# Kernel tuning notes

Hardware: AMD Instinct MI355X
Metric: run time of the kernel (lower is better)

## Reference

```python
import jax, jax.numpy as jnp
import numpy as np

B, S, T, E, H, F = 2, 2048, 2048, 1024, 16, 4096
HD = E // H
EPS = 1e-5


def setup_inputs() -> dict:
    key = jax.random.key(0)
    ks = jax.random.split(key, 16)
    def w(k, shape):
        return (jax.random.normal(k, shape, jnp.float32) * 0.02)
    d = {
        "x": jax.random.normal(ks[0], (B, S, E), jnp.float32),
        "enc": jax.random.normal(ks[1], (B, T, E), jnp.float32),
    }
    for i, n in enumerate(["sa_q", "sa_k", "sa_v", "sa_o", "ca_q", "ca_k", "ca_v", "ca_o"]):
        d[n + "w"] = w(ks[2 + i], (E, E))  # torch Linear: [out, in]
        d[n + "b"] = jnp.zeros((E,), jnp.float32)
    d["w1"] = w(ks[10], (F, E)); d["b1"] = jnp.zeros((F,), jnp.float32)
    d["w2"] = w(ks[11], (E, F)); d["b2"] = jnp.zeros((E,), jnp.float32)
    for n in ["ln1", "ln2", "ln3"]:
        d[n + "_g"] = jnp.ones((E,), jnp.float32)
        d[n + "_b"] = jnp.zeros((E,), jnp.float32)
    return d


def _layernorm(x, g, b):
    m = jnp.mean(x, axis=-1, keepdims=True)
    v = jnp.mean((x - m) ** 2, axis=-1, keepdims=True)
    return (x - m) / jnp.sqrt(v + EPS) * g + b


def _heads(x, w, b):
    bsz, sl, _ = x.shape
    y = x @ w.T + b
    return y.reshape(bsz, sl, H, HD).transpose(0, 2, 1, 3)  # [B,H,S,hd]


def _mha(xq, xkv, qw, qb, kw, kb, vw, vb, ow, ob, causal):
    q = _heads(xq, qw, qb)
    k = _heads(xkv, kw, kb)
    v = _heads(xkv, vw, vb)
    scores = jnp.einsum('bhsd,bhtd->bhst', q, k) / np.sqrt(HD).astype(np.float32)
    if causal:
        sl, tl = scores.shape[-2], scores.shape[-1]
        mask = jnp.tril(jnp.ones((sl, tl), bool))
        scores = jnp.where(mask, scores, -jnp.inf)
    a = jax.nn.softmax(scores, axis=-1)
    o = jnp.einsum('bhst,bhtd->bhsd', a, v)
    o = o.transpose(0, 2, 1, 3).reshape(xq.shape[0], xq.shape[1], E)
    return o @ ow.T + ob


def reference(x, enc,
              sa_qw, sa_qb, sa_kw, sa_kb, sa_vw, sa_vb, sa_ow, sa_ob,
              ca_qw, ca_qb, ca_kw, ca_kb, ca_vw, ca_vb, ca_ow, ca_ob,
              w1, b1, w2, b2,
              ln1_g, ln1_b, ln2_g, ln2_b, ln3_g, ln3_b):
    sa = _mha(x, x, sa_qw, sa_qb, sa_kw, sa_kb, sa_vw, sa_vb, sa_ow, sa_ob, True)
    x = _layernorm(x + sa, ln1_g, ln1_b)
    ca = _mha(x, enc, ca_qw, ca_qb, ca_kw, ca_kb, ca_vw, ca_vb, ca_ow, ca_ob, False)
    x = _layernorm(x + ca, ln2_g, ln2_b)
    ffn = jax.nn.relu(x @ w1.T + b1) @ w2.T + b2
    return _layernorm(x + ffn, ln3_g, ln3_b)
```

## Files before the change

### kernel.cpp

```cpp
#include <hip/hip_runtime.h>
#include <hip/hip_bf16.h>
#include <stdint.h>

typedef __attribute__((ext_vector_type(8))) short s16x8;
typedef __attribute__((ext_vector_type(4))) short s16x4;
typedef __attribute__((ext_vector_type(4))) float f32x4;

#define DEV static __device__ __forceinline__

DEV ushort f2bu(float f){
  unsigned u = __builtin_bit_cast(unsigned, f);
  return (ushort)((u + 0x7fffu + ((u >> 16) & 1u)) >> 16);
}
DEV ushort f2bn(float f){
  return __builtin_bit_cast(ushort, __float2bfloat16(f));
}

DEV void gload16(const void* g, void* l){
  __builtin_amdgcn_global_load_lds((const __attribute__((address_space(1))) void*)g,
                                   (__attribute__((address_space(3))) void*)l, 16, 0, 0);
}

struct ConvArgs {
  const float* src[17];
  void*        dst[17];
  int blk_end[17];
  int nel[17];
  unsigned f32mask;
};

__global__ void __launch_bounds__(256) k_conv(ConvArgs a){
  int bi = blockIdx.x, seg = 0;
  while (bi >= a.blk_end[seg]) seg++;
  int b0 = seg ? a.blk_end[seg-1] : 0;
  long off = (long)(bi - b0)*2048 + (long)threadIdx.x*8;
  if (off >= a.nel[seg]) return;
  const float* s = a.src[seg] + off;
  f32x4 v0 = *(const f32x4*)s;
  f32x4 v1 = *(const f32x4*)(s+4);
  if ((a.f32mask >> seg) & 1u){
    float* d = (float*)a.dst[seg] + off;
    *(f32x4*)d = v0; *(f32x4*)(d+4) = v1;
  } else {
    ushort* d = (ushort*)a.dst[seg] + off;
    s16x8 o;
#pragma unroll
    for (int j = 0; j < 4; j++){ o[j] = (short)f2bu(v0[j]); o[4+j] = (short)f2bu(v1[j]); }
    *(s16x8*)d = o;
  }
}

template<int MODE, bool DBUF>
__global__ void __launch_bounds__(256) k_gemm(const ushort* __restrict__ A, const ushort* __restrict__ W,
    const float* __restrict__ bias, float* __restrict__ Cf, ushort* __restrict__ Cb,
    int M, int N, int Kext, int lda, int ldb, long long sstride)
{
  constexpr int NB = DBUF ? 2 : 1;
  __shared__ __align__(16) ushort lsA[NB][128*64];
  __shared__ __align__(16) ushort lsB[NB][128*64];
  const int t = threadIdx.x, w = t >> 6, u = t & 63, lr = u & 15, lk = u >> 4;
  const int m0 = blockIdx.y * 128, n0 = blockIdx.x * 128;
  const int s = blockIdx.z;
  const int wm = w >> 1, wn = w & 1;
  const int rA = t >> 3, c8 = (t & 7) * 8;
  const ushort* Ap = A + (size_t)(m0 + rA) * lda + (size_t)s * Kext + c8;
  const ushort* Wp = W + (size_t)(n0 + rA) * ldb + (size_t)s * Kext + c8;
  if (s){ bias = nullptr; if (Cf) Cf += sstride; }
  f32x4 acc[4][4] = {};
  const int nk = Kext >> 6;

  auto stage = [&](int k0, int buf){
#pragma unroll
    for (int j = 0; j < 4; j++){
      gload16(Ap + (size_t)j*32*lda + k0, &lsA[buf][0] + j*2048 + w*512);
      gload16(Wp + (size_t)j*32*ldb + k0, &lsB[buf][0] + j*2048 + w*512);
    }
  };
  auto body = [&](const ushort* La, const ushort* Lb){
#pragma unroll
    for (int ks = 0; ks < 2; ks++){
      s16x8 af[4], bfr[4];
#pragma unroll
      for (int i = 0; i < 4; i++) af[i]  = *(const s16x8*)(La + (wm*64 + i*16 + lr)*64 + ks*32 + lk*8);
#pragma unroll
      for (int i = 0; i < 4; i++) bfr[i] = *(const s16x8*)(Lb + (wn*64 + i*16 + lr)*64 + ks*32 + lk*8);
#pragma unroll
      for (int mi = 0; mi < 4; mi++)
#pragma unroll
        for (int ni = 0; ni < 4; ni++)
          acc[mi][ni] = __builtin_amdgcn_mfma_f32_16x16x32_bf16(af[mi], bfr[ni], acc[mi][ni], 0, 0, 0);
    }
  };

  if (DBUF){
    stage(0, 0);
    for (int tk = 0; tk < nk; ++tk){
      __syncthreads();
      if (tk + 1 < nk) stage((tk + 1) << 6, (tk + 1) & 1);
      body(&lsA[tk & 1][0], &lsB[tk & 1][0]);
    }
  } else {
    for (int tk = 0; tk < nk; ++tk){
      stage(tk << 6, 0);
      __syncthreads();
      body(&lsA[0][0], &lsB[0][0]);
      __syncthreads();
    }
  }

#pragma unroll
  for (int mi = 0; mi < 4; mi++){
#pragma unroll
    for (int ni = 0; ni < 4; ni++){
      const int row = m0 + wm*64 + mi*16 + lk*4;
      const int col = n0 + wn*64 + ni*16 + lr;
      const float bv = bias ? bias[col] : 0.f;
#pragma unroll
      for (int i = 0; i < 4; i++){
        float v = acc[mi][ni][i] + bv;
        if (MODE == 2) v = fmaxf(v, 0.f);
        size_t idx = (size_t)(row + i) * N + col;
        if (MODE == 1) Cf[idx] = v; else Cb[idx] = f2bn(v);
      }
    }
  }
}

__global__ void __launch_bounds__(256) k_vt(const ushort* __restrict__ V, ushort* __restrict__ Vt,
                                            int stride, int S)
{
  __shared__ ushort tile[64][72];
  const int st = blockIdx.x*64, h = blockIdx.y, b = blockIdx.z;
  const int r = threadIdx.x >> 3, c8 = (threadIdx.x & 7)*8;
#pragma unroll
  for (int j = 0; j < 2; j++){
    int s = r + j*32;
    s16x8 v = *(const s16x8*)(V + (size_t)(b*S + st + s)*stride + h*64 + c8);
    *(s16x8*)&tile[s][c8] = v;
  }
  __syncthreads();
#pragma unroll
  for (int j = 0; j < 2; j++){
    int d = r + j*32;
    s16x8 o;
#pragma unroll
    for (int e = 0; e < 8; e++) o[e] = tile[c8+e][d];
    *(s16x8*)(Vt + ((size_t)((b*16 + h)*64 + d))*S + st + c8) = o;
  }
}

template<bool CAUSAL>
__global__ void __launch_bounds__(512) k_attn(const ushort* __restrict__ Q, const ushort* __restrict__ Kg,
    const ushort* __restrict__ Vt, ushort* __restrict__ O, int sQ, int sK, int SQ, int SKV)
{
  __shared__ __align__(16) ushort Kl[2][64*64];
  __shared__ __align__(16) ushort Vl[2][64*64];
  __shared__ __align__(16) ushort Pl[8][16*64];
  const int t = threadIdx.x, w = t >> 6, u = t & 63, lr = u & 15, lk = u >> 4;
  const int hb = blockIdx.x;
  const int b = hb >> 4, h = hb & 15;
  const int qt = CAUSAL ? (gridDim.y - 1 - blockIdx.y) : blockIdx.y;
  const int q0 = qt * 128;

  const ushort* qp = Q + (size_t)(b*SQ + q0 + w*16 + lr) * sQ + h*64 + lk*8;
  s16x8 qf0 = *(const s16x8*)qp;
  s16x8 qf1 = *(const s16x8*)(qp + 32);

  f32x4 oacc[4] = {};
  float mrun = -1e30f, lrun = 0.f;

  const int nkt = CAUSAL ? (2*qt + 2) : (SKV >> 6);
  const int srow = t >> 3;
  const int scol = t & 7;

  const size_t kvbase = (size_t)b * SKV;
  const size_t vtbase = (size_t)((b*16 + h)*64);

  auto stage = [&](int kt, int buf){
    gload16(Kg + (kvbase + kt*64 + srow)*sK + h*64 + 8*(scol ^ (srow & 7)), &Kl[buf][0] + w*512);
    gload16(Vt + (vtbase + srow)*SKV + kt*64 + 8*(scol ^ (srow & 7)), &Vl[buf][0] + w*512);
  };

  stage(0, 0);
  __syncthreads();

  char* Pc = (char*)&Pl[w][0];
  const int swzq = (lr & 7) << 4;

  for (int kt = 0; kt < nkt; kt++){
    const int buf = kt & 1;
    if (kt + 1 < nkt) stage(kt + 1, buf ^ 1);
    char* Kc = (char*)&Kl[buf][0];
    char* Vc = (char*)&Vl[buf][0];

    f32x4 sacc[4] = {};
#pragma unroll
    for (int ks = 0; ks < 2; ks++){
      s16x8 qf = ks ? qf1 : qf0;
#pragma unroll
      for (int ni = 0; ni < 4; ni++){
        int key = ni*16 + lr;
        s16x8 kf = *(const s16x8*)(Kc + key*128 + ((ks*64 + lk*16) ^ ((key & 7) << 4)));
        sacc[ni] = __builtin_amdgcn_mfma_f32_16x16x32_bf16(kf, qf, sacc[ni], 0, 0, 0);
      }
    }
    if (CAUSAL && kt >= 2*qt){
      const int koff = kt*64 - q0;
#pragma unroll
      for (int ni = 0; ni < 4; ni++)
#pragma unroll
        for (int i = 0; i < 4; i++)
          if (koff + 16*ni + lk*4 + i > w*16 + lr) sacc[ni][i] = -1e30f;
    }

    const float c = 0.18033688f;
    float mx = fmaxf(fmaxf(fmaxf(sacc[0][0],sacc[0][1]), fmaxf(sacc[0][2],sacc[0][3])),
                     fmaxf(fmaxf(sacc[1][0],sacc[1][1]), fmaxf(sacc[1][2],sacc[1][3])));
    mx = fmaxf(mx, fmaxf(fmaxf(sacc[2][0],sacc[2][1]), fmaxf(sacc[2][2],sacc[2][3])));
    mx = fmaxf(mx, fmaxf(fmaxf(sacc[3][0],sacc[3][1]), fmaxf(sacc[3][2],sacc[3][3])));
    mx = fmaxf(mx, __shfl_xor(mx, 16));
    mx = fmaxf(mx, __shfl_xor(mx, 32));
    float mn = fmaxf(mrun, mx);
    float sc = __builtin_exp2f((mrun - mn) * c);
    mrun = mn;
    float rs = 0.f;
#pragma unroll
    for (int ni = 0; ni < 4; ni++)
#pragma unroll
      for (int i = 0; i < 4; i++){
        float p = __builtin_exp2f((sacc[ni][i] - mn) * c);
        sacc[ni][i] = p; rs += p;
      }
    rs += __shfl_xor(rs, 16);
    rs += __shfl_xor(rs, 32);
    lrun = lrun * sc + rs;

#pragma unroll
    for (int ni = 0; ni < 4; ni++){
      s16x4 pk;
#pragma unroll
      for (int i = 0; i < 4; i++) pk[i] = (short)f2bn(sacc[ni][i]);
      *(s16x4*)(Pc + lr*128 + ((32*ni + 8*lk) ^ swzq)) = pk;
    }

    float scO[4];
#pragma unroll
    for (int i = 0; i < 4; i++) scO[i] = __shfl(sc, lk*4 + i);
#pragma unroll
    for (int ni = 0; ni < 4; ni++)
#pragma unroll
      for (int i = 0; i < 4; i++) oacc[ni][i] *= scO[i];

#pragma unroll
    for (int ks = 0; ks < 2; ks++){
      s16x8 pf = *(const s16x8*)(Pc + lr*128 + ((ks*64 + lk*16) ^ swzq));
#pragma unroll
      for (int ni = 0; ni < 4; ni++){
        int d = ni*16 + lr;
        s16x8 vf = *(const s16x8*)(Vc + d*128 + ((ks*64 + lk*16) ^ ((d & 7) << 4)));
        oacc[ni] = __builtin_amdgcn_mfma_f32_16x16x32_bf16(pf, vf, oacc[ni], 0, 0, 0);
      }
    }
    __syncthreads();
  }

  float il = 1.f / lrun;
  float invl[4];
#pragma unroll
  for (int i = 0; i < 4; i++) invl[i] = __shfl(il, lk*4 + i);
#pragma unroll
  for (int ni = 0; ni < 4; ni++)
#pragma unroll
    for (int i = 0; i < 4; i++)
      O[(size_t)(b*SQ + q0 + w*16 + lk*4 + i)*1024 + h*64 + ni*16 + lr] = f2bn(oacc[ni][i] * invl[i]);
}

template<bool WB16>
__global__ void __launch_bounds__(256) k_ln(const float* __restrict__ R, const float* __restrict__ P,
    const float* __restrict__ P2, const float* __restrict__ G, const float* __restrict__ Bv,
    float* __restrict__ Of, ushort* __restrict__ Ob)
{
  const int row = blockIdx.x, t = threadIdx.x, w = t >> 6, u = t & 63;
  const size_t base = (size_t)row * 1024 + t * 4;
  f32x4 r = *(const f32x4*)(R + base);
  f32x4 p = *(const f32x4*)(P + base);
  f32x4 v = r + p;
  if (P2){ f32x4 p2 = *(const f32x4*)(P2 + base); v += p2; }
  float s = 0.f, q = 0.f;
#pragma unroll
  for (int j = 0; j < 4; j++){ s += v[j]; q += v[j]*v[j]; }
#pragma unroll
  for (int md = 1; md < 64; md <<= 1){ s += __shfl_xor(s, md); q += __shfl_xor(q, md); }
  __shared__ float ps[4], pq[4];
  if (u == 0){ ps[w] = s; pq[w] = q; }
  __syncthreads();
  s = ps[0] + ps[1] + ps[2] + ps[3];
  q = pq[0] + pq[1] + pq[2] + pq[3];
  const float mean = s * (1.f/1024.f);
  const float var  = q * (1.f/1024.f) - mean*mean;
  const float rstd = rsqrtf(var + 1e-5f);
  f32x4 g4 = *(const f32x4*)(G  + t*4);
  f32x4 b4 = *(const f32x4*)(Bv + t*4);
  f32x4 o;
#pragma unroll
  for (int j = 0; j < 4; j++) o[j] = (v[j] - mean) * rstd * g4[j] + b4[j];
  *(f32x4*)(Of + base) = o;
  if (WB16){
    s16x4 ob;
#pragma unroll
    for (int j = 0; j < 4; j++) ob[j] = (short)f2bn(o[j]);
    *(s16x4*)(Ob + base) = ob;
  }
}

extern "C" void kernel_launch(void* const* d_in, const int* in_sizes, int n_in,
                              void* d_out, int out_size, void* d_ws, size_t ws_size,
                              hipStream_t stream)
{
  const float* x   = (const float*)d_in[0];
  const float* enc = (const float*)d_in[1];
  const float* aw[8]; const float* ab[8];
  for (int i = 0; i < 8; i++){ aw[i] = (const float*)d_in[2 + 2*i]; ab[i] = (const float*)d_in[3 + 2*i]; }
  const float* w1 = (const float*)d_in[18]; const float* b1 = (const float*)d_in[19];
  const float* w2 = (const float*)d_in[20]; const float* b2 = (const float*)d_in[21];
  const float* lg[3] = {(const float*)d_in[22], (const float*)d_in[24], (const float*)d_in[26]};
  const float* lb[3] = {(const float*)d_in[23], (const float*)d_in[25], (const float*)d_in[27]};
  float* out = (float*)d_out;

  const size_t MB = 1024ull * 1024ull;
  if (ws_size < 129 * MB) return;
  char* ws = (char*)d_ws;
  ushort* wqkv = (ushort*)(ws + 0*MB);
  ushort* wcq  = (ushort*)(ws + 6*MB);
  ushort* wkv  = (ushort*)(ws + 8*MB);
  ushort* wo1w = (ushort*)(ws + 12*MB);
  ushort* wo2w = (ushort*)(ws + 14*MB);
  ushort* w1b  = (ushort*)(ws + 16*MB);
  ushort* w2b  = (ushort*)(ws + 24*MB);
  ushort* xb   = (ushort*)(ws + 32*MB);
  ushort* encb = (ushort*)(ws + 40*MB);
  ushort* attb = (ushort*)(ws + 48*MB);
  float*  proj = (float*)(ws + 56*MB);
  float*  x1f  = (float*)(ws + 72*MB);
  ushort* xab  = (ushort*)(ws + 88*MB);
  ushort* QKVb    = (ushort*)(ws + 96*MB);
  ushort* Vt1     = (ushort*)(ws + 120*MB);
  ushort* crossQb = (ushort*)(ws + 96*MB);
  ushort* encKVb  = (ushort*)(ws + 104*MB);
  ushort* Vt2     = (ushort*)(ws + 120*MB);
  ushort* hb      = (ushort*)(ws + 96*MB);
  float*  proj2wo  = (float*)(ws + 96*MB);
  float*  proj2ffn = (float*)(ws + 32*MB);
  float*  bqkv = (float*)(ws + 128*MB);
  float*  bkv  = (float*)(ws + 128*MB + 16384);

  const long long ssWO  = ((long long)(96 - 56) * (long long)MB) / 4;
  const long long ssFFN = ((long long)(32 - 56) * (long long)MB) / 4;

  ConvArgs ca;
  const float* srcs[17] = { x, enc, aw[0], aw[1], aw[2], aw[3], aw[4], aw[5], aw[6], aw[7],
                            w1, w2, ab[0], ab[1], ab[2], ab[5], ab[6] };
  void* dsts[17] = { xb, encb, wqkv, wqkv + 1048576, wqkv + 2097152, wo1w, wcq, wkv, wkv + 1048576, wo2w,
                     w1b, w2b, bqkv, bqkv + 1024, bqkv + 2048, bkv, bkv + 1024 };
  int nels[17] = { 4194304, 4194304, 1048576, 1048576, 1048576, 1048576, 1048576, 1048576, 1048576, 1048576,
                   4194304, 4194304, 1024, 1024, 1024, 1024, 1024 };
  int acc_blk = 0;
  for (int i = 0; i < 17; i++){
    ca.src[i] = srcs[i]; ca.dst[i] = dsts[i]; ca.nel[i] = nels[i];
    acc_blk += (nels[i] + 2047) / 2048;
    ca.blk_end[i] = acc_blk;
  }
  ca.f32mask = 0x1F000u;
  k_conv<<<acc_blk, 256, 0, stream>>>(ca);

  auto gemm = [&](const ushort* A, const ushort* W, const float* bias, float* Cf, ushort* Cb,
                  int M, int N, int Kext, int lda, int ldb, int mode, bool dbuf,
                  int nsplit, long long sstride){
    dim3 g(N/128, M/128, nsplit);
    if (dbuf){
      if (mode == 0)      k_gemm<0,true ><<<g, 256, 0, stream>>>(A, W, bias, Cf, Cb, M, N, Kext, lda, ldb, sstride);
      else if (mode == 1) k_gemm<1,true ><<<g, 256, 0, stream>>>(A, W, bias, Cf, Cb, M, N, Kext, lda, ldb, sstride);
      else                k_gemm<2,true ><<<g, 256, 0, stream>>>(A, W, bias, Cf, Cb, M, N, Kext, lda, ldb, sstride);
    } else {
      if (mode == 0)      k_gemm<0,false><<<g, 256, 0, stream>>>(A, W, bias, Cf, Cb, M, N, Kext, lda, ldb, sstride);
      else if (mode == 1) k_gemm<1,false><<<g, 256, 0, stream>>>(A, W, bias, Cf, Cb, M, N, Kext, lda, ldb, sstride);
      else                k_gemm<2,false><<<g, 256, 0, stream>>>(A, W, bias, Cf, Cb, M, N, Kext, lda, ldb, sstride);
    }
  };

  gemm(xb, wqkv, bqkv, nullptr, QKVb, 4096, 3072, 1024, 1024, 1024, 0, false, 1, 0);
  k_vt<<<dim3(32,16,2), 256, 0, stream>>>(QKVb + 2048, Vt1, 3072, 2048);
  k_attn<true><<<dim3(32,16), 512, 0, stream>>>(QKVb, QKVb + 1024, Vt1, attb, 3072, 3072, 2048, 2048);
  gemm(attb, wo1w, ab[3], proj, nullptr, 4096, 1024, 512, 1024, 1024, 1, true, 2, ssWO);
  k_ln<true><<<4096, 256, 0, stream>>>(x, proj, proj2wo, lg[0], lb[0], x1f, xab);

  gemm(xab,  wcq, ab[4], nullptr, crossQb, 4096, 1024, 1024, 1024, 1024, 0, true, 1, 0);
  gemm(encb, wkv, bkv,   nullptr, encKVb,  4096, 2048, 1024, 1024, 1024, 0, false, 1, 0);
  k_vt<<<dim3(32,16,2), 256, 0, stream>>>(encKVb + 1024, Vt2, 2048, 2048);
  k_attn<false><<<dim3(32,16), 512, 0, stream>>>(crossQb, encKVb, Vt2, attb, 1024, 2048, 2048, 2048);
  gemm(attb, wo2w, ab[7], proj, nullptr, 4096, 1024, 512, 1024, 1024, 1, true, 2, ssWO);
  k_ln<true><<<4096, 256, 0, stream>>>(x1f, proj, proj2wo, lg[1], lb[1], x1f, xab);

  gemm(xab, w1b, b1, nullptr, hb, 4096, 4096, 1024, 1024, 1024, 2, false, 1, 0);
  gemm(hb,  w2b, b2, proj, nullptr, 4096, 1024, 2048, 4096, 4096, 1, true, 2, ssFFN);
  k_ln<false><<<4096, 256, 0, stream>>>(x1f, proj, proj2ffn, lg[2], lb[2], out, nullptr);
}
```

Measured before the change: 448.9 us.

## Add 256x256-tile double-buffered GEMM kernel for large projections

Adds a new GEMM kernel with 256x256 output tiles, 512 threads, double-buffered LDS filled by direct global-to-LDS loads, an XOR-swizzled LDS layout, a workgroup-ID swizzle for L2 locality, and split phases that interleave prefetch with MFMA blocks under raised wave priority. It replaces the 128x128 GEMM for the QKV, encoder KV and FFN-up projections. The goal is more data reuse per tile and overlap of loads with compute. The cost is fewer workgroups (128–256), which may underfill the CUs, plus heavy register and LDS use that limits occupancy to one block.

```diff
diff --git a/kernel.cpp b/kernel.cpp
--- a/kernel.cpp
+++ b/kernel.cpp
@@ -113,6 +113,141 @@
 #pragma unroll
     for (int ni = 0; ni < 4; ni++){
       const int row = m0 + wm*64 + mi*16 + lk*4;
+      const int col = n0 + wn*64 + ni*16 + lr;
+      const float bv = bias ? bias[col] : 0.f;
+#pragma unroll
+      for (int i = 0; i < 4; i++){
+        float v = acc[mi][ni][i] + bv;
+        if (MODE == 2) v = fmaxf(v, 0.f);
+        size_t idx = (size_t)(row + i) * N + col;
+        if (MODE == 1) Cf[idx] = v; else Cb[idx] = f2bn(v);
+      }
+    }
+  }
+}
+
+template<int MODE>
+__global__ void __launch_bounds__(512, 1) k_gemm256(const ushort* __restrict__ A, const ushort* __restrict__ W,
+    const float* __restrict__ bias, float* __restrict__ Cf, ushort* __restrict__ Cb,
+    int N, int K, int lda, int ldb)
+{
+  __shared__ __align__(16) ushort lsA[2][256*64];
+  __shared__ __align__(16) ushort lsB[2][256*64];
+  const int t = threadIdx.x, w = t >> 6, u = t & 63, lr = u & 15, lk = u >> 4;
+  const int gx = gridDim.x;
+  const int nwg = gx * gridDim.y;
+  const int id = blockIdx.y * gx + blockIdx.x;
+  const int swz = (id & 7) * (nwg >> 3) + (id >> 3);
+  const int n0 = (swz % gx) * 256, m0 = (swz / gx) * 256;
+  const int wm = w >> 2, wn = w & 3;
+
+  const int r0 = w*8 + (u >> 3), cc = u & 7;
+  const int csw = 8 * (cc ^ (r0 & 7));
+  const ushort* Ap = A + (size_t)(m0 + r0) * lda + csw;
+  const ushort* Wp = W + (size_t)(n0 + r0) * ldb + csw;
+
+  f32x4 acc[8][4] = {};
+  const int nt = K >> 6;
+  const int swl = lr & 7;
+  s16x8 afr[4], bfr[4];
+
+#pragma unroll
+  for (int j = 0; j < 4; j++){
+    gload16(Ap + (size_t)(64*j)*lda, &lsA[0][0] + w*512 + j*4096);
+    gload16(Wp + (size_t)(64*j)*ldb, &lsB[0][0] + w*512 + j*4096);
+  }
+  asm volatile("s_waitcnt vmcnt(0)" ::: "memory");
+  __builtin_amdgcn_s_barrier();
+
+  for (int tk = 0; tk < nt; ++tk){
+    const char* La = (const char*)&lsA[tk & 1][0];
+    const char* Lb = (const char*)&lsB[tk & 1][0];
+    ushort* dA = &lsA[(tk & 1) ^ 1][0] + w*512;
+    ushort* dB = &lsB[(tk & 1) ^ 1][0] + w*512;
+    const bool pf = (tk + 1 < nt);
+    const size_t k1 = (size_t)(tk + 1) << 6;
+
+#pragma unroll
+    for (int i = 0; i < 4; i++)
+      afr[i] = *(const s16x8*)(La + (wm*128 + i*16 + lr)*128 + ((lk ^ swl) * 16));
+#pragma unroll
+    for (int i = 0; i < 4; i++)
+      bfr[i] = *(const s16x8*)(Lb + (wn*64 + i*16 + lr)*128 + ((lk ^ swl) * 16));
+    if (pf){
+      gload16(Ap + k1, dA);
+      gload16(Wp + k1, dB);
+      gload16(Ap + (size_t)64*lda + k1, dA + 4096);
+      gload16(Wp + (size_t)64*ldb + k1, dB + 4096);
+    }
+    __builtin_amdgcn_s_barrier();
+    asm volatile("s_waitcnt lgkmcnt(0)" ::: "memory");
+    __builtin_amdgcn_s_setprio(1);
+#pragma unroll
+    for (int mi = 0; mi < 4; mi++)
+#pragma unroll
+      for (int ni = 0; ni < 4; ni++)
+        acc[mi][ni] = __builtin_amdgcn_mfma_f32_16x16x32_bf16(afr[mi], bfr[ni], acc[mi][ni], 0, 0, 0);
+    __builtin_amdgcn_s_setprio(0);
+    __builtin_amdgcn_s_barrier();
+
+#pragma unroll
+    for (int i = 0; i < 4; i++)
+      afr[i] = *(const s16x8*)(La + (wm*128 + 64 + i*16 + lr)*128 + ((lk ^ swl) * 16));
+    if (pf){
+      gload16(Ap + (size_t)128*lda + k1, dA + 8192);
+      gload16(Wp + (size_t)128*ldb + k1, dB + 8192);
+      gload16(Ap + (size_t)192*lda + k1, dA + 12288);
+      gload16(Wp + (size_t)192*ldb + k1, dB + 12288);
+    }
+    __builtin_amdgcn_s_barrier();
+    asm volatile("s_waitcnt lgkmcnt(0)" ::: "memory");
+    __builtin_amdgcn_s_setprio(1);
+#pragma unroll
+    for (int mi = 0; mi < 4; mi++)
+#pragma unroll
+      for (int ni = 0; ni < 4; ni++)
+        acc[4+mi][ni] = __builtin_amdgcn_mfma_f32_16x16x32_bf16(afr[mi], bfr[ni], acc[4+mi][ni], 0, 0, 0);
+    __builtin_amdgcn_s_setprio(0);
+    __builtin_amdgcn_s_barrier();
+
+#pragma unroll
+    for (int i = 0; i < 4; i++)
+      afr[i] = *(const s16x8*)(La + (wm*128 + i*16 + lr)*128 + (((4 + lk) ^ swl) * 16));
+#pragma unroll
+    for (int i = 0; i < 4; i++)
+      bfr[i] = *(const s16x8*)(Lb + (wn*64 + i*16 + lr)*128 + (((4 + lk) ^ swl) * 16));
+    __builtin_amdgcn_s_barrier();
+    asm volatile("s_waitcnt lgkmcnt(0)" ::: "memory");
+    __builtin_amdgcn_s_setprio(1);
+#pragma unroll
+    for (int mi = 0; mi < 4; mi++)
+#pragma unroll
+      for (int ni = 0; ni < 4; ni++)
+        acc[mi][ni] = __builtin_amdgcn_mfma_f32_16x16x32_bf16(afr[mi], bfr[ni], acc[mi][ni], 0, 0, 0);
+    __builtin_amdgcn_s_setprio(0);
+    __builtin_amdgcn_s_barrier();
+
+#pragma unroll
+    for (int i = 0; i < 4; i++)
+      afr[i] = *(const s16x8*)(La + (wm*128 + 64 + i*16 + lr)*128 + (((4 + lk) ^ swl) * 16));
+    __builtin_amdgcn_s_barrier();
+    asm volatile("s_waitcnt lgkmcnt(0)" ::: "memory");
+    __builtin_amdgcn_s_setprio(1);
+#pragma unroll
+    for (int mi = 0; mi < 4; mi++)
+#pragma unroll
+      for (int ni = 0; ni < 4; ni++)
+        acc[4+mi][ni] = __builtin_amdgcn_mfma_f32_16x16x32_bf16(afr[mi], bfr[ni], acc[4+mi][ni], 0, 0, 0);
+    __builtin_amdgcn_s_setprio(0);
+    asm volatile("s_waitcnt vmcnt(0)" ::: "memory");
+    __builtin_amdgcn_s_barrier();
+  }
+
+#pragma unroll
+  for (int mi = 0; mi < 8; mi++){
+#pragma unroll
+    for (int ni = 0; ni < 4; ni++){
+      const int row = m0 + wm*128 + mi*16 + lk*4;
       const int col = n0 + wn*64 + ni*16 + lr;
       const float bv = bias ? bias[col] : 0.f;
 #pragma unroll
@@ -388,20 +523,20 @@
     }
   };
 
-  gemm(xb, wqkv, bqkv, nullptr, QKVb, 4096, 3072, 1024, 1024, 1024, 0, false, 1, 0);
+  k_gemm256<0><<<dim3(12,16), 512, 0, stream>>>(xb, wqkv, bqkv, nullptr, QKVb, 3072, 1024, 1024, 1024);
   k_vt<<<dim3(32,16,2), 256, 0, stream>>>(QKVb + 2048, Vt1, 3072, 2048);
   k_attn<true><<<dim3(32,16), 512, 0, stream>>>(QKVb, QKVb + 1024, Vt1, attb, 3072, 3072, 2048, 2048);
   gemm(attb, wo1w, ab[3], proj, nullptr, 4096, 1024, 512, 1024, 1024, 1, true, 2, ssWO);
   k_ln<true><<<4096, 256, 0, stream>>>(x, proj, proj2wo, lg[0], lb[0], x1f, xab);
 
   gemm(xab,  wcq, ab[4], nullptr, crossQb, 4096, 1024, 1024, 1024, 1024, 0, true, 1, 0);
-  gemm(encb, wkv, bkv,   nullptr, encKVb,  4096, 2048, 1024, 1024, 1024, 0, false, 1, 0);
+  k_gemm256<0><<<dim3(8,16), 512, 0, stream>>>(encb, wkv, bkv, nullptr, encKVb, 2048, 1024, 1024, 1024);
   k_vt<<<dim3(32,16,2), 256, 0, stream>>>(encKVb + 1024, Vt2, 2048, 2048);
   k_attn<false><<<dim3(32,16), 512, 0, stream>>>(crossQb, encKVb, Vt2, attb, 1024, 2048, 2048, 2048);
   gemm(attb, wo2w, ab[7], proj, nullptr, 4096, 1024, 512, 1024, 1024, 1, true, 2, ssWO);
   k_ln<true><<<4096, 256, 0, stream>>>(x1f, proj, proj2wo, lg[1], lb[1], x1f, xab);
 
-  gemm(xab, w1b, b1, nullptr, hb, 4096, 4096, 1024, 1024, 1024, 2, false, 1, 0);
+  k_gemm256<2><<<dim3(16,16), 512, 0, stream>>>(xab, w1b, b1, nullptr, hb, 4096, 1024, 1024, 1024);
   gemm(hb,  w2b, b2, proj, nullptr, 4096, 1024, 2048, 4096, 4096, 1, true, 2, ssFFN);
   k_ln<false><<<4096, 256, 0, stream>>>(x1f, proj, proj2ffn, lg[2], lb[2], out, nullptr);
 }
```

Result: faster. 426.8 us (-4.9%).
